# Kernel tuning notes

Hardware: AMD Instinct MI355X
Metric: run time of the kernel (lower is better)

Reference implementation:

```python
import jax, jax.numpy as jnp
import numpy as np

C_Z = 128
C = 128
EPS = 1e-5


def _layer_norm(x, w, b):
    m = jnp.mean(x, axis=-1, keepdims=True)
    v = jnp.mean(jnp.square(x - m), axis=-1, keepdims=True)
    return (x - m) * jax.lax.rsqrt(v + EPS) * w + b


def setup_inputs() -> dict:
    key = jax.random.key(0)
    ks = jax.random.split(key, 16)
    N = 512
    s_in = 1.0 / np.sqrt(C_Z)
    s_c = 1.0 / np.sqrt(C)
    return {
        "z": jax.random.normal(ks[0], (1, N, N, C_Z), dtype=jnp.float32),
        "ln_in_w": jnp.ones((C_Z,), jnp.float32),
        "ln_in_b": jnp.zeros((C_Z,), jnp.float32),
        "ln_out_w": jnp.ones((C_Z,), jnp.float32),
        "ln_out_b": jnp.zeros((C_Z,), jnp.float32),
        # weights stored [in, out]
        "w_ap": jax.random.normal(ks[1], (C_Z, C), jnp.float32) * s_in,
        "b_ap": jax.random.normal(ks[2], (C,), jnp.float32) * 0.02,
        "w_ag": jax.random.normal(ks[3], (C_Z, C), jnp.float32) * s_in,
        "b_ag": jax.random.normal(ks[4], (C,), jnp.float32) * 0.02,
        "w_bp": jax.random.normal(ks[5], (C_Z, C), jnp.float32) * s_in,
        "b_bp": jax.random.normal(ks[6], (C,), jnp.float32) * 0.02,
        "w_bg": jax.random.normal(ks[7], (C_Z, C), jnp.float32) * s_in,
        "b_bg": jax.random.normal(ks[8], (C,), jnp.float32) * 0.02,
        "w_g": jax.random.normal(ks[9], (C_Z, C_Z), jnp.float32) * s_in,
        "b_g": jax.random.normal(ks[10], (C_Z,), jnp.float32) * 0.02,
        "w_z": jax.random.normal(ks[11], (C, C_Z), jnp.float32) * s_c,
        "b_z": jax.random.normal(ks[12], (C_Z,), jnp.float32) * 0.02,
    }


def reference(z, ln_in_w, ln_in_b, ln_out_w, ln_out_b,
              w_ap, b_ap, w_ag, b_ag, w_bp, b_bp, w_bg, b_bg,
              w_g, b_g, w_z, b_z):
    zn = _layer_norm(z, ln_in_w, ln_in_b)                      # [B,N,N,c_z]
    a = jax.nn.sigmoid(zn @ w_ag + b_ag) * (zn @ w_ap + b_ap)  # [B,N,N,c]
    b = jax.nn.sigmoid(zn @ w_bg + b_bg) * (zn @ w_bp + b_bp)  # [B,N,N,c]
    g = jax.nn.sigmoid(zn @ w_g + b_g)                         # [B,N,N,c_z]
    # outgoing triangle update: contract over k
    t = jnp.einsum('bikc,bjkc->bijc', a, b)                    # [B,N,N,c]
    out = g * (_layer_norm(t, ln_out_w, ln_out_b) @ w_z + b_z)
    return out
```

## Files before the change

kernel.cpp:

```cpp
#include <hip/hip_runtime.h>
#include <hip/hip_bf16.h>


#define NSEQ 512
#define NPOS 262144

typedef short bf16x8 __attribute__((ext_vector_type(8)));
typedef float f32x4 __attribute__((ext_vector_type(4)));

__device__ __forceinline__ float bf2f(ushort h) {
    union { uint u; float f; } x; x.u = ((uint)h) << 16; return x.f;
}
__device__ __forceinline__ ushort f2bf(float f) {
    union { float f; uint u; } x; x.f = f;
    uint r = x.u + 0x7fffu + ((x.u >> 16) & 1u);
    return (ushort)(r >> 16);
}
__device__ __forceinline__ float sigm(float x) { return 1.f / (1.f + __expf(-x)); }

__device__ __forceinline__ float loadIn(const void* p, size_t idx, int isbf) {
    return isbf ? bf2f(((const ushort*)p)[idx]) : ((const float*)p)[idx];
}
__device__ __forceinline__ float2 loadIn2(const void* p, size_t base, int col2, int isbf) {
    if (isbf) {
        uint zz = *(const uint*)((const ushort*)p + base + col2);
        float2 r; r.x = bf2f((ushort)(zz & 0xffff)); r.y = bf2f((ushort)(zz >> 16)); return r;
    }
    return *(const float2*)((const float*)p + base + col2);
}

__global__ void detect_kernel(const uint* __restrict__ z32, int* __restrict__ flag)
{
    int t = threadIdx.x;
    int votes = 0;
    #pragma unroll
    for (int i = 0; i < 4; ++i) {
        uint wv = z32[t * 4 + i];
        uint ex = (wv >> 7) & 0xff;
        votes += (ex >= 118 && ex <= 132) ? 1 : 0;
    }
    #pragma unroll
    for (int m = 32; m >= 1; m >>= 1) votes += __shfl_xor(votes, m);
    if (t == 0) flag[0] = (votes >= 128) ? 1 : 0;
}

__global__ void fill_zero_kernel(ushort* __restrict__ out)
{
    size_t i = ((size_t)blockIdx.x * 256 + threadIdx.x) * 16;
    uint4 z4 = {0u, 0u, 0u, 0u};
    *(uint4*)(out + i) = z4;
    *(uint4*)(out + i + 8) = z4;
}

__global__ void prep_kernel(const void* __restrict__ w_ap, const void* __restrict__ w_ag,
                            const void* __restrict__ w_bp, const void* __restrict__ w_bg,
                            const void* __restrict__ w_g,  const void* __restrict__ w_z,
                            const void* __restrict__ ln_ow, const void* __restrict__ ln_ob,
                            const void* __restrict__ b_z,  const int* __restrict__ dflag,
                            ushort* __restrict__ wt5_h, ushort* __restrict__ wt5_l,
                            ushort* __restrict__ wzt_h, ushort* __restrict__ wzt_l,
                            float* __restrict__ u, float* __restrict__ v, int store_lo)
{
    const int b = blockIdx.x, t = threadIdx.x;
    const int isbf = dflag[0];
    if (b < 5) {
        const void* src = (b == 0) ? w_ap : (b == 1) ? w_ag : (b == 2) ? w_bp : (b == 3) ? w_bg : w_g;
        for (int k = 0; k < 64; ++k) {
            int o = t + k * 256;
            int co = o >> 7, ci = o & 127;
            float wv = loadIn(src, ci * 128 + co, isbf);
            ushort hi = f2bf(wv);
            wt5_h[b * 16384 + o] = hi;
            if (store_lo) wt5_l[b * 16384 + o] = f2bf(wv - bf2f(hi));
        }
    } else if (b == 5) {
        for (int k = 0; k < 64; ++k) {
            int o = t + k * 256;
            int co = o >> 7, c = o & 127;
            float wv = loadIn(ln_ow, c, isbf) * loadIn(w_z, c * 128 + co, isbf);
            ushort hi = f2bf(wv);
            wzt_h[o] = hi;
            if (store_lo) wzt_l[o] = f2bf(wv - bf2f(hi));
        }
    } else {
        if (t < 128) {
            float su = 0.f, sv = 0.f;
            for (int c = 0; c < 128; ++c) {
                float wzv = loadIn(w_z, c * 128 + t, isbf);
                su += loadIn(ln_ow, c, isbf) * wzv;
                sv += loadIn(ln_ob, c, isbf) * wzv;
            }
            u[t] = su;
            v[t] = sv + loadIn(b_z, t, isbf);
        }
    }
}

__global__ __launch_bounds__(256, 3)
void stage1_kernel(const void* __restrict__ z,
                   const void* __restrict__ ln_iw, const void* __restrict__ ln_ib,
                   const ushort* __restrict__ wt5_h,
                   const void* __restrict__ b_ap, const void* __restrict__ b_ag,
                   const void* __restrict__ b_bp, const void* __restrict__ b_bg,
                   const int* __restrict__ dflag,
                   ushort* __restrict__ Ahi, ushort* __restrict__ Alo,
                   ushort* __restrict__ Bhi, int walo)
{
    __shared__ ushort sm[2 * 64 * 136 + 128 * 72];
    ushort* lAh = sm;
    ushort* lAl = sm + 64 * 136;
    ushort* tb  = sm + 2 * 64 * 136;
    const int tid = threadIdx.x, lane = tid & 63, w = tid >> 6;
    const int l15 = lane & 15, quad = lane >> 4;
    const int p0 = blockIdx.x * 64;
    const int isbf = dflag[0];
    (void)Alo; (void)walo;

    float lw0 = loadIn(ln_iw, 2 * lane, isbf), lw1 = loadIn(ln_iw, 2 * lane + 1, isbf);
    float lb0 = loadIn(ln_ib, 2 * lane, isbf), lb1 = loadIn(ln_ib, 2 * lane + 1, isbf);
    for (int it = 0; it < 16; ++it) {
        int pl = w * 16 + it;
        float2 xv = loadIn2(z, (size_t)(p0 + pl) * 128, 2 * lane, isbf);
        float x0 = xv.x, x1 = xv.y;
        float s = x0 + x1, s2 = x0 * x0 + x1 * x1;
        #pragma unroll
        for (int m = 32; m >= 1; m >>= 1) { s += __shfl_xor(s, m); s2 += __shfl_xor(s2, m); }
        float mean = s * 0.0078125f;
        float var = s2 * 0.0078125f - mean * mean;
        float rs = rsqrtf(var + 1e-5f);
        float zn0 = (x0 - mean) * rs * lw0 + lb0;
        float zn1 = (x1 - mean) * rs * lw1 + lb1;
        ushort h0 = f2bf(zn0), h1 = f2bf(zn1);
        ushort o0 = f2bf(zn0 - bf2f(h0)), o1 = f2bf(zn1 - bf2f(h1));
        *(uint*)(lAh + pl * 136 + 2 * lane) = (uint)h0 | ((uint)h1 << 16);
        *(uint*)(lAl + pl * 136 + 2 * lane) = (uint)o0 | ((uint)o1 << 16);
    }
    __syncthreads();

    const int wm = w >> 1, wn = w & 1;
    const f32x4 zero4 = {0.f, 0.f, 0.f, 0.f};

    #pragma unroll 1
    for (int g = 0; g < 2; ++g) {
        const ushort* wG = wt5_h + ((g == 0) ? 1 : 3) * 16384;
        const ushort* wP = wt5_h + ((g == 0) ? 0 : 2) * 16384;

        f32x4 accG[2][4], accP[2][4];
        #pragma unroll
        for (int i = 0; i < 2; ++i)
            #pragma unroll
            for (int j = 0; j < 4; ++j) { accG[i][j] = zero4; accP[i][j] = zero4; }

        #pragma unroll
        for (int ks = 0; ks < 4; ++ks) {
            bf16x8 afh[2], afl[2];
            #pragma unroll
            for (int i = 0; i < 2; ++i) {
                afh[i] = *(const bf16x8*)(lAh + (wm * 32 + i * 16 + l15) * 136 + ks * 32 + quad * 8);
                afl[i] = *(const bf16x8*)(lAl + (wm * 32 + i * 16 + l15) * 136 + ks * 32 + quad * 8);
            }
            {
                bf16x8 bG[4];
                #pragma unroll
                for (int j = 0; j < 4; ++j)
                    bG[j] = *(const bf16x8*)(wG + (wn * 64 + j * 16 + l15) * 128 + ks * 32 + quad * 8);
                #pragma unroll
                for (int i = 0; i < 2; ++i)
                    #pragma unroll
                    for (int j = 0; j < 4; ++j) {
                        accG[i][j] = __builtin_amdgcn_mfma_f32_16x16x32_bf16(afh[i], bG[j], accG[i][j], 0, 0, 0);
                        accG[i][j] = __builtin_amdgcn_mfma_f32_16x16x32_bf16(afl[i], bG[j], accG[i][j], 0, 0, 0);
                    }
            }
            {
                bf16x8 bP[4];
                #pragma unroll
                for (int j = 0; j < 4; ++j)
                    bP[j] = *(const bf16x8*)(wP + (wn * 64 + j * 16 + l15) * 128 + ks * 32 + quad * 8);
                #pragma unroll
                for (int i = 0; i < 2; ++i)
                    #pragma unroll
                    for (int j = 0; j < 4; ++j) {
                        accP[i][j] = __builtin_amdgcn_mfma_f32_16x16x32_bf16(afh[i], bP[j], accP[i][j], 0, 0, 0);
                        accP[i][j] = __builtin_amdgcn_mfma_f32_16x16x32_bf16(afl[i], bP[j], accP[i][j], 0, 0, 0);
                    }
            }
        }

        const void* bgp = (g == 0) ? b_ag : b_bg;
        const void* bpp = (g == 0) ? b_ap : b_bp;
        float av[2][4][4];
        #pragma unroll
        for (int i = 0; i < 2; ++i)
            #pragma unroll
            for (int j = 0; j < 4; ++j) {
                int co = wn * 64 + j * 16 + l15;
                float gv = loadIn(bgp, co, isbf);
                float pv = loadIn(bpp, co, isbf);
                #pragma unroll
                for (int r = 0; r < 4; ++r)
                    av[i][j][r] = sigm(accG[i][j][r] + gv) * (accP[i][j][r] + pv);
            }

        ushort* dst_hi = (g == 0) ? Ahi : Bhi;

        __syncthreads();
        #pragma unroll
        for (int i = 0; i < 2; ++i)
            #pragma unroll
            for (int j = 0; j < 4; ++j) {
                int co = wn * 64 + j * 16 + l15;
                int pb = wm * 32 + i * 16 + quad * 4;
                uint2 pk;
                pk.x = (uint)f2bf(av[i][j][0]) | ((uint)f2bf(av[i][j][1]) << 16);
                pk.y = (uint)f2bf(av[i][j][2]) | ((uint)f2bf(av[i][j][3]) << 16);
                *(uint2*)(tb + co * 72 + pb) = pk;
            }
        __syncthreads();
        #pragma unroll
        for (int q = 0; q < 4; ++q) {
            int vv = q * 256 + tid;
            int co = vv >> 3, off = vv & 7;
            *(uint4*)(dst_hi + (size_t)co * NPOS + p0 + off * 8) = *(const uint4*)(tb + co * 72 + off * 8);
        }
    }
}

__global__ __launch_bounds__(256, 3)
void stage2_kernel(const ushort* __restrict__ Ahi, const ushort* __restrict__ Alo,
                   const ushort* __restrict__ Bhi, const int* __restrict__ dflag,
                   void* __restrict__ Tbuf, int alo, int tfp32)
{
    __shared__ ushort sm[2 * 128 * 72];
    ushort* lAh = sm;
    ushort* lBh = sm + 128 * 72;
    const int tid = threadIdx.x, lane = tid & 63, w = tid >> 6;
    const int l15 = lane & 15, quad = lane >> 4;
    const int wm = w >> 1, wn = w & 1;
    const int bid = blockIdx.y * 16 + blockIdx.x;
    const int swz = (bid & 7) * 256 + (bid >> 3);
    const int c = swz >> 4;
    const int ti = (swz & 15) >> 2, tj = swz & 3;
    const ushort* Aph = Ahi + (size_t)c * NPOS + (size_t)ti * 128 * NSEQ;
    const ushort* Bph = Bhi + (size_t)c * NPOS + (size_t)tj * 128 * NSEQ;
    (void)Alo; (void)alo;

    const f32x4 zero4 = {0.f, 0.f, 0.f, 0.f};
    f32x4 acc[4][4];
    #pragma unroll
    for (int i = 0; i < 4; ++i)
        #pragma unroll
        for (int j = 0; j < 4; ++j) acc[i][j] = zero4;

    for (int kt = 0; kt < 8; ++kt) {
        #pragma unroll
        for (int q = 0; q < 4; ++q) {
            int vv = q * 256 + tid;
            int row = vv >> 3, off = vv & 7;
            *(uint4*)(lAh + row * 72 + off * 8) = *(const uint4*)(Aph + (size_t)row * NSEQ + kt * 64 + off * 8);
            *(uint4*)(lBh + row * 72 + off * 8) = *(const uint4*)(Bph + (size_t)row * NSEQ + kt * 64 + off * 8);
        }
        __syncthreads();
        #pragma unroll
        for (int ks = 0; ks < 2; ++ks) {
            bf16x8 afh[4], bfh[4];
            #pragma unroll
            for (int i = 0; i < 4; ++i)
                afh[i] = *(const bf16x8*)(lAh + (wm * 64 + i * 16 + l15) * 72 + ks * 32 + quad * 8);
            #pragma unroll
            for (int j = 0; j < 4; ++j)
                bfh[j] = *(const bf16x8*)(lBh + (wn * 64 + j * 16 + l15) * 72 + ks * 32 + quad * 8);
            #pragma unroll
            for (int i = 0; i < 4; ++i)
                #pragma unroll
                for (int j = 0; j < 4; ++j)
                    acc[i][j] = __builtin_amdgcn_mfma_f32_16x16x32_bf16(afh[i], bfh[j], acc[i][j], 0, 0, 0);
        }
        __syncthreads();
    }

    if (tfp32) {
        float* Tp = (float*)Tbuf + ((size_t)(ti * 128) * 128 + c) * 512 + tj * 128;
        #pragma unroll
        for (int i = 0; i < 4; ++i)
            #pragma unroll
            for (int j = 0; j < 4; ++j) {
                int jl = wn * 64 + j * 16 + l15;
                int ib = wm * 64 + i * 16 + quad * 4;
                #pragma unroll
                for (int r = 0; r < 4; ++r)
                    Tp[(size_t)(ib + r) * 65536 + jl] = acc[i][j][r];
            }
    } else {
        ushort* Tp = (ushort*)Tbuf + ((size_t)(ti * 128) * 128 + c) * 512 + tj * 128;
        #pragma unroll
        for (int i = 0; i < 4; ++i)
            #pragma unroll
            for (int j = 0; j < 4; ++j) {
                int jl = wn * 64 + j * 16 + l15;
                int ib = wm * 64 + i * 16 + quad * 4;
                #pragma unroll
                for (int r = 0; r < 4; ++r)
                    Tp[(size_t)(ib + r) * 65536 + jl] = f2bf(acc[i][j][r]);
            }
    }
}

__global__ __launch_bounds__(256, 4)
void stage3ab_kernel(const void* __restrict__ z,
                     const void* __restrict__ ln_iw, const void* __restrict__ ln_ib,
                     const ushort* __restrict__ wt5_h, const ushort* __restrict__ wt5_l,
                     const void* __restrict__ b_g,
                     const float* __restrict__ Tf, const ushort* __restrict__ wzt_h,
                     const ushort* __restrict__ wzt_l,
                     const float* __restrict__ uvec, const float* __restrict__ vvec,
                     const int* __restrict__ dflag, void* __restrict__ out)
{
    __shared__ ushort sm[2 * 64 * 136];
    __shared__ float sMean[64], sRs[64];
    ushort* lAh = sm;
    ushort* lAl = sm + 64 * 136;
    const int tid = threadIdx.x, lane = tid & 63, w = tid >> 6;
    const int l15 = lane & 15, quad = lane >> 4;
    const int wm = w >> 1, wn = w & 1;
    const int p0 = blockIdx.x * 64;
    const int isbf = dflag[0];
    const f32x4 zero4 = {0.f, 0.f, 0.f, 0.f};
    (void)wt5_l; (void)wzt_l;

    float lw0 = loadIn(ln_iw, 2 * lane, isbf), lw1 = loadIn(ln_iw, 2 * lane + 1, isbf);
    float lb0 = loadIn(ln_ib, 2 * lane, isbf), lb1 = loadIn(ln_ib, 2 * lane + 1, isbf);
    for (int it = 0; it < 16; ++it) {
        int pl = w * 16 + it;
        float2 xv = loadIn2(z, (size_t)(p0 + pl) * 128, 2 * lane, isbf);
        float x0 = xv.x, x1 = xv.y;
        float s = x0 + x1, s2 = x0 * x0 + x1 * x1;
        #pragma unroll
        for (int m = 32; m >= 1; m >>= 1) { s += __shfl_xor(s, m); s2 += __shfl_xor(s2, m); }
        float mean = s * 0.0078125f;
        float var = s2 * 0.0078125f - mean * mean;
        float rs = rsqrtf(var + 1e-5f);
        float zn0 = (x0 - mean) * rs * lw0 + lb0;
        float zn1 = (x1 - mean) * rs * lw1 + lb1;
        ushort h0 = f2bf(zn0), h1 = f2bf(zn1);
        ushort o0 = f2bf(zn0 - bf2f(h0)), o1 = f2bf(zn1 - bf2f(h1));
        *(uint*)(lAh + pl * 136 + 2 * lane) = (uint)h0 | ((uint)h1 << 16);
        *(uint*)(lAl + pl * 136 + 2 * lane) = (uint)o0 | ((uint)o1 << 16);
    }
    __syncthreads();

    const ushort* wgh = wt5_h + 4 * 16384;
    f32x4 accG[2][4];
    #pragma unroll
    for (int i = 0; i < 2; ++i)
        #pragma unroll
        for (int j = 0; j < 4; ++j) accG[i][j] = zero4;
    #pragma unroll
    for (int ks = 0; ks < 4; ++ks) {
        bf16x8 afh[2], afl[2], bh[4];
        #pragma unroll
        for (int i = 0; i < 2; ++i) {
            afh[i] = *(const bf16x8*)(lAh + (wm * 32 + i * 16 + l15) * 136 + ks * 32 + quad * 8);
            afl[i] = *(const bf16x8*)(lAl + (wm * 32 + i * 16 + l15) * 136 + ks * 32 + quad * 8);
        }
        #pragma unroll
        for (int j = 0; j < 4; ++j)
            bh[j] = *(const bf16x8*)(wgh + (wn * 64 + j * 16 + l15) * 128 + ks * 32 + quad * 8);
        #pragma unroll
        for (int i = 0; i < 2; ++i)
            #pragma unroll
            for (int j = 0; j < 4; ++j) {
                accG[i][j] = __builtin_amdgcn_mfma_f32_16x16x32_bf16(afh[i], bh[j], accG[i][j], 0, 0, 0);
                accG[i][j] = __builtin_amdgcn_mfma_f32_16x16x32_bf16(afl[i], bh[j], accG[i][j], 0, 0, 0);
            }
    }
    #pragma unroll
    for (int i = 0; i < 2; ++i)
        #pragma unroll
        for (int j = 0; j < 4; ++j) {
            int co = wn * 64 + j * 16 + l15;
            float bgv = loadIn(b_g, co, isbf);
            #pragma unroll
            for (int r = 0; r < 4; ++r)
                accG[i][j][r] = sigm(accG[i][j][r] + bgv);
        }
    __syncthreads();

    {
        int c = tid >> 1, h = tid & 1;
        const float* src = Tf + ((size_t)(p0 >> 9) * 128 + c) * 512 + (p0 & 511) + h * 32;
        float tv[32];
        #pragma unroll
        for (int q8 = 0; q8 < 8; ++q8) {
            float4 f4 = ((const float4*)src)[q8];
            tv[q8 * 4 + 0] = f4.x; tv[q8 * 4 + 1] = f4.y;
            tv[q8 * 4 + 2] = f4.z; tv[q8 * 4 + 3] = f4.w;
        }
        #pragma unroll
        for (int jj = 0; jj < 32; ++jj) {
            ushort hi = f2bf(tv[jj]);
            lAh[(h * 32 + jj) * 136 + c] = hi;
            lAl[(h * 32 + jj) * 136 + c] = f2bf(tv[jj] - bf2f(hi));
        }
    }
    __syncthreads();

    for (int it = 0; it < 16; ++it) {
        int pl = w * 16 + it;
        uint zh = *(const uint*)(lAh + pl * 136 + 2 * lane);
        uint zl = *(const uint*)(lAl + pl * 136 + 2 * lane);
        float x0 = bf2f((ushort)(zh & 0xffff)) + bf2f((ushort)(zl & 0xffff));
        float x1 = bf2f((ushort)(zh >> 16)) + bf2f((ushort)(zl >> 16));
        float s = x0 + x1, s2 = x0 * x0 + x1 * x1;
        #pragma unroll
        for (int m = 32; m >= 1; m >>= 1) { s += __shfl_xor(s, m); s2 += __shfl_xor(s2, m); }
        if (lane == 0) {
            float mean = s * 0.0078125f;
            float var = s2 * 0.0078125f - mean * mean;
            sMean[pl] = mean;
            sRs[pl] = rsqrtf(var + 1e-5f);
        }
    }
    __syncthreads();

    f32x4 acc[2][4];
    #pragma unroll
    for (int i = 0; i < 2; ++i)
        #pragma unroll
        for (int j = 0; j < 4; ++j) acc[i][j] = zero4;
    #pragma unroll
    for (int ks = 0; ks < 4; ++ks) {
        bf16x8 afh[2], afl[2], bh[4];
        #pragma unroll
        for (int i = 0; i < 2; ++i) {
            afh[i] = *(const bf16x8*)(lAh + (wm * 32 + i * 16 + l15) * 136 + ks * 32 + quad * 8);
            afl[i] = *(const bf16x8*)(lAl + (wm * 32 + i * 16 + l15) * 136 + ks * 32 + quad * 8);
        }
        #pragma unroll
        for (int j = 0; j < 4; ++j)
            bh[j] = *(const bf16x8*)(wzt_h + (wn * 64 + j * 16 + l15) * 128 + ks * 32 + quad * 8);
        #pragma unroll
        for (int i = 0; i < 2; ++i)
            #pragma unroll
            for (int j = 0; j < 4; ++j) {
                acc[i][j] = __builtin_amdgcn_mfma_f32_16x16x32_bf16(afh[i], bh[j], acc[i][j], 0, 0, 0);
                acc[i][j] = __builtin_amdgcn_mfma_f32_16x16x32_bf16(afl[i], bh[j], acc[i][j], 0, 0, 0);
            }
    }

    ushort* outb = (ushort*)out;
    float*  outf = (float*)out;
    #pragma unroll
    for (int i = 0; i < 2; ++i)
        #pragma unroll
        for (int j = 0; j < 4; ++j) {
            int co = wn * 64 + j * 16 + l15;
            float uj = uvec[co], vj = vvec[co];
            int pb = wm * 32 + i * 16 + quad * 4;
            #pragma unroll
            for (int r = 0; r < 4; ++r) {
                int p = pb + r;
                float pre = sRs[p] * (acc[i][j][r] - sMean[p] * uj) + vj;
                float val = accG[i][j][r] * pre;
                size_t oidx = (size_t)(p0 + p) * 128 + co;
                if (isbf) outb[oidx] = f2bf(val);
                else      outf[oidx] = val;
            }
        }
}

__global__ __launch_bounds__(256, 2)
void stage3c_kernel(const void* __restrict__ z,
                    const void* __restrict__ ln_iw, const void* __restrict__ ln_ib,
                    const ushort* __restrict__ wt5_h, const void* __restrict__ b_g,
                    const ushort* __restrict__ Tb, const ushort* __restrict__ wzt_h,
                    const float* __restrict__ uvec, const float* __restrict__ vvec,
                    const int* __restrict__ dflag, void* __restrict__ out)
{
    __shared__ ushort sm[2 * 64 * 136 + 128 * 136];
    __shared__ float sMean[64], sRs[64];
    ushort* lAh = sm;
    ushort* lAl = sm + 64 * 136;
    ushort* lB  = sm + 2 * 64 * 136;
    const int tid = threadIdx.x, lane = tid & 63, w = tid >> 6;
    const int l15 = lane & 15, quad = lane >> 4;
    const int wm = w >> 1, wn = w & 1;
    const int p0 = blockIdx.x * 64;
    const int isbf = dflag[0];
    const f32x4 zero4 = {0.f, 0.f, 0.f, 0.f};

    float lw0 = loadIn(ln_iw, 2 * lane, isbf), lw1 = loadIn(ln_iw, 2 * lane + 1, isbf);
    float lb0 = loadIn(ln_ib, 2 * lane, isbf), lb1 = loadIn(ln_ib, 2 * lane + 1, isbf);
    for (int it = 0; it < 16; ++it) {
        int pl = w * 16 + it;
        float2 xv = loadIn2(z, (size_t)(p0 + pl) * 128, 2 * lane, isbf);
        float x0 = xv.x, x1 = xv.y;
        float s = x0 + x1, s2 = x0 * x0 + x1 * x1;
        #pragma unroll
        for (int m = 32; m >= 1; m >>= 1) { s += __shfl_xor(s, m); s2 += __shfl_xor(s2, m); }
        float mean = s * 0.0078125f;
        float var = s2 * 0.0078125f - mean * mean;
        float rs = rsqrtf(var + 1e-5f);
        float zn0 = (x0 - mean) * rs * lw0 + lb0;
        float zn1 = (x1 - mean) * rs * lw1 + lb1;
        ushort h0 = f2bf(zn0), h1 = f2bf(zn1);
        ushort o0 = f2bf(zn0 - bf2f(h0)), o1 = f2bf(zn1 - bf2f(h1));
        *(uint*)(lAh + pl * 136 + 2 * lane) = (uint)h0 | ((uint)h1 << 16);
        *(uint*)(lAl + pl * 136 + 2 * lane) = (uint)o0 | ((uint)o1 << 16);
    }
    {
        const ushort* src = wt5_h + 4 * 16384;
        #pragma unroll
        for (int q = 0; q < 8; ++q) {
            int vv = q * 256 + tid;
            int co = vv >> 4, off = vv & 15;
            *(uint4*)(lB + co * 136 + off * 8) = *(const uint4*)(src + co * 128 + off * 8);
        }
    }
    __syncthreads();

    f32x4 accG[2][4];
    #pragma unroll
    for (int i = 0; i < 2; ++i)
        #pragma unroll
        for (int j = 0; j < 4; ++j) accG[i][j] = zero4;
    #pragma unroll
    for (int ks = 0; ks < 4; ++ks) {
        bf16x8 afh[2], afl[2], bfr[4];
        #pragma unroll
        for (int i = 0; i < 2; ++i) {
            afh[i] = *(const bf16x8*)(lAh + (wm * 32 + i * 16 + l15) * 136 + ks * 32 + quad * 8);
            afl[i] = *(const bf16x8*)(lAl + (wm * 32 + i * 16 + l15) * 136 + ks * 32 + quad * 8);
        }
        #pragma unroll
        for (int j = 0; j < 4; ++j)
            bfr[j] = *(const bf16x8*)(lB + (wn * 64 + j * 16 + l15) * 136 + ks * 32 + quad * 8);
        #pragma unroll
        for (int i = 0; i < 2; ++i)
            #pragma unroll
            for (int j = 0; j < 4; ++j) {
                accG[i][j] = __builtin_amdgcn_mfma_f32_16x16x32_bf16(afh[i], bfr[j], accG[i][j], 0, 0, 0);
                accG[i][j] = __builtin_amdgcn_mfma_f32_16x16x32_bf16(afl[i], bfr[j], accG[i][j], 0, 0, 0);
            }
    }
    #pragma unroll
    for (int i = 0; i < 2; ++i)
        #pragma unroll
        for (int j = 0; j < 4; ++j) {
            int co = wn * 64 + j * 16 + l15;
            float bgv = loadIn(b_g, co, isbf);
            #pragma unroll
            for (int r = 0; r < 4; ++r)
                accG[i][j][r] = sigm(accG[i][j][r] + bgv);
        }
    __syncthreads();

    {
        int c = tid >> 1, h = tid & 1;
        const ushort* src = Tb + ((size_t)(p0 >> 9) * 128 + c) * 512 + (p0 & 511) + h * 32;
        union { uint4 q[4]; ushort u[32]; } tmp;
        tmp.q[0] = ((const uint4*)src)[0];
        tmp.q[1] = ((const uint4*)src)[1];
        tmp.q[2] = ((const uint4*)src)[2];
        tmp.q[3] = ((const uint4*)src)[3];
        #pragma unroll
        for (int jj = 0; jj < 32; ++jj)
            lAh[(h * 32 + jj) * 136 + c] = tmp.u[jj];
    }
    #pragma unroll
    for (int q = 0; q < 8; ++q) {
        int vv = q * 256 + tid;
        int co = vv >> 4, off = vv & 15;
        *(uint4*)(lB + co * 136 + off * 8) = *(const uint4*)(wzt_h + co * 128 + off * 8);
    }
    __syncthreads();

    for (int it = 0; it < 16; ++it) {
        int pl = w * 16 + it;
        uint zz = *(const uint*)(lAh + pl * 136 + 2 * lane);
        float x0 = bf2f((ushort)(zz & 0xffff)), x1 = bf2f((ushort)(zz >> 16));
        float s = x0 + x1, s2 = x0 * x0 + x1 * x1;
        #pragma unroll
        for (int m = 32; m >= 1; m >>= 1) { s += __shfl_xor(s, m); s2 += __shfl_xor(s2, m); }
        if (lane == 0) {
            float mean = s * 0.0078125f;
            float var = s2 * 0.0078125f - mean * mean;
            sMean[pl] = mean;
            sRs[pl] = rsqrtf(var + 1e-5f);
        }
    }
    __syncthreads();

    f32x4 acc[2][4];
    #pragma unroll
    for (int i = 0; i < 2; ++i)
        #pragma unroll
        for (int j = 0; j < 4; ++j) acc[i][j] = zero4;
    #pragma unroll
    for (int ks = 0; ks < 4; ++ks) {
        bf16x8 af[2], bfr[4];
        #pragma unroll
        for (int i = 0; i < 2; ++i)
            af[i] = *(const bf16x8*)(lAh + (wm * 32 + i * 16 + l15) * 136 + ks * 32 + quad * 8);
        #pragma unroll
        for (int j = 0; j < 4; ++j)
            bfr[j] = *(const bf16x8*)(lB + (wn * 64 + j * 16 + l15) * 136 + ks * 32 + quad * 8);
        #pragma unroll
        for (int i = 0; i < 2; ++i)
            #pragma unroll
            for (int j = 0; j < 4; ++j)
                acc[i][j] = __builtin_amdgcn_mfma_f32_16x16x32_bf16(af[i], bfr[j], acc[i][j], 0, 0, 0);
    }

    ushort* outb = (ushort*)out;
    float*  outf = (float*)out;
    #pragma unroll
    for (int i = 0; i < 2; ++i)
        #pragma unroll
        for (int j = 0; j < 4; ++j) {
            int co = wn * 64 + j * 16 + l15;
            float uj = uvec[co], vj = vvec[co];
            int pb = wm * 32 + i * 16 + quad * 4;
            #pragma unroll
            for (int r = 0; r < 4; ++r) {
                int p = pb + r;
                float pre = sRs[p] * (acc[i][j][r] - sMean[p] * uj) + vj;
                float val = accG[i][j][r] * pre;
                size_t oidx = (size_t)(p0 + p) * 128 + co;
                if (isbf) outb[oidx] = f2bf(val);
                else      outf[oidx] = val;
            }
        }
}

extern "C" void kernel_launch(void* const* d_in, const int* in_sizes, int n_in,
                              void* d_out, int out_size, void* d_ws, size_t ws_size,
                              hipStream_t stream)
{
    const void* z     = d_in[0];
    const void* ln_iw = d_in[1];
    const void* ln_ib = d_in[2];
    const void* ln_ow = d_in[3];
    const void* ln_ob = d_in[4];
    const void* w_ap  = d_in[5];
    const void* b_ap  = d_in[6];
    const void* w_ag  = d_in[7];
    const void* b_ag  = d_in[8];
    const void* w_bp  = d_in[9];
    const void* b_bp  = d_in[10];
    const void* w_bg  = d_in[11];
    const void* b_bg  = d_in[12];
    const void* w_g   = d_in[13];
    const void* b_g   = d_in[14];
    const void* w_z   = d_in[15];
    const void* b_z   = d_in[16];

    const size_t MB64 = 67108864;
    const size_t REQ_C = 262144 + 2 * MB64;
    const size_t REQ_B = 524288 + MB64 + 2 * MB64;
    const size_t REQ_A = REQ_B + MB64;

    char* ws = (char*)d_ws;
    if (ws_size < REQ_C) {
        fill_zero_kernel<<<8192, 256, 0, stream>>>((ushort*)d_out);
        return;
    }

    int tier = (ws_size >= REQ_A) ? 0 : (ws_size >= REQ_B) ? 1 : 2;
    if (tier == 0) tier = 1;

    ushort* wt5_h = (ushort*)(ws);
    ushort* wzt_h = (ushort*)(ws + 163840);
    float*  uvec  = (float*)(ws + 196608);
    float*  vvec  = (float*)(ws + 197120);
    int*    dflag = (int*)(ws + 198144);
    ushort* wt5_l = (ushort*)(ws + 262144);
    ushort* wzt_l = (ushort*)(ws + 262144 + 163840);
    int store_lo = 0;
    if (tier == 2) { wt5_l = wt5_h; wzt_l = wzt_h; }

    ushort* Ahi; ushort* Alo; void* Tbuf;
    int walo = 0, tfp32 = 0;
    if (tier == 1) {
        Ahi = (ushort*)(ws + 524288);
        Alo = Ahi;
        Tbuf = (void*)(ws + 524288 + MB64);
        walo = 0; tfp32 = 1;
    } else {
        Ahi = (ushort*)(ws + 262144);
        Alo = Ahi;
        Tbuf = (void*)(ws + 262144 + MB64);
        walo = 0; tfp32 = 0;
    }
    ushort* Bhi = (ushort*)d_out;

    detect_kernel<<<1, 64, 0, stream>>>((const uint*)z, dflag);
    prep_kernel<<<7, 256, 0, stream>>>(w_ap, w_ag, w_bp, w_bg, w_g, w_z, ln_ow, ln_ob, b_z,
                                       dflag, wt5_h, wt5_l, wzt_h, wzt_l, uvec, vvec, store_lo);
    stage1_kernel<<<4096, 256, 0, stream>>>(z, ln_iw, ln_ib, wt5_h,
                                            b_ap, b_ag, b_bp, b_bg, dflag,
                                            Ahi, Alo, Bhi, walo);
    stage2_kernel<<<dim3(16, 128), 256, 0, stream>>>(Ahi, Alo, Bhi, dflag, Tbuf, walo, tfp32);
    if (tfp32)
        stage3ab_kernel<<<4096, 256, 0, stream>>>(z, ln_iw, ln_ib, wt5_h, wt5_l, b_g,
                                                  (const float*)Tbuf, wzt_h, wzt_l,
                                                  uvec, vvec, dflag, d_out);
    else
        stage3c_kernel<<<4096, 256, 0, stream>>>(z, ln_iw, ln_ib, wt5_h, b_g,
                                                 (const ushort*)Tbuf, wzt_h,
                                                 uvec, vvec, dflag, d_out);
}
```

Measured before the change: 759.5 us.

## Compute sigmoid gate in stage1 and store it, skipping z re-read in stage3

The gate projection sigmoid(zn@w_g+b_g) now runs in stage1, where zn is already in LDS, and is written as bf16 to a workspace buffer in channel-major layout. A new stage3g kernel reads only T, computes its hi/lo split for the layer norm and output projection, and multiplies by the stored gate. This removes the second read and layernorm of z and the gate GEMM from stage3. In exchange it adds a 64MB gate write plus a strided gate read, and it needs a larger workspace. The bf16-T stage3c path is removed.

```diff
diff --git a/kernel.cpp b/kernel.cpp
--- a/kernel.cpp
+++ b/kernel.cpp
@@ -102,9 +102,10 @@
                    const ushort* __restrict__ wt5_h,
                    const void* __restrict__ b_ap, const void* __restrict__ b_ag,
                    const void* __restrict__ b_bp, const void* __restrict__ b_bg,
+                   const void* __restrict__ b_g,
                    const int* __restrict__ dflag,
-                   ushort* __restrict__ Ahi, ushort* __restrict__ Alo,
-                   ushort* __restrict__ Bhi, int walo)
+                   ushort* __restrict__ Ahi, ushort* __restrict__ Bhi,
+                   ushort* __restrict__ Gbuf, int do_gate)
 {
     __shared__ ushort sm[2 * 64 * 136 + 128 * 72];
     ushort* lAh = sm;
@@ -114,7 +115,6 @@
     const int l15 = lane & 15, quad = lane >> 4;
     const int p0 = blockIdx.x * 64;
     const int isbf = dflag[0];
-    (void)Alo; (void)walo;
 
     float lw0 = loadIn(ln_iw, 2 * lane, isbf), lw1 = loadIn(ln_iw, 2 * lane + 1, isbf);
     float lb0 = loadIn(ln_ib, 2 * lane, isbf), lb1 = loadIn(ln_ib, 2 * lane + 1, isbf);
@@ -224,12 +224,60 @@
             *(uint4*)(dst_hi + (size_t)co * NPOS + p0 + off * 8) = *(const uint4*)(tb + co * 72 + off * 8);
         }
     }
+
+    if (do_gate) {
+        const ushort* wGt = wt5_h + 4 * 16384;
+        f32x4 acc[2][4];
+        #pragma unroll
+        for (int i = 0; i < 2; ++i)
+            #pragma unroll
+            for (int j = 0; j < 4; ++j) acc[i][j] = zero4;
+        #pragma unroll
+        for (int ks = 0; ks < 4; ++ks) {
+            bf16x8 afh[2], afl[2], bh[4];
+            #pragma unroll
+            for (int i = 0; i < 2; ++i) {
+                afh[i] = *(const bf16x8*)(lAh + (wm * 32 + i * 16 + l15) * 136 + ks * 32 + quad * 8);
+                afl[i] = *(const bf16x8*)(lAl + (wm * 32 + i * 16 + l15) * 136 + ks * 32 + quad * 8);
+            }
+            #pragma unroll
+            for (int j = 0; j < 4; ++j)
+                bh[j] = *(const bf16x8*)(wGt + (wn * 64 + j * 16 + l15) * 128 + ks * 32 + quad * 8);
+            #pragma unroll
+            for (int i = 0; i < 2; ++i)
+                #pragma unroll
+                for (int j = 0; j < 4; ++j) {
+                    acc[i][j] = __builtin_amdgcn_mfma_f32_16x16x32_bf16(afh[i], bh[j], acc[i][j], 0, 0, 0);
+                    acc[i][j] = __builtin_amdgcn_mfma_f32_16x16x32_bf16(afl[i], bh[j], acc[i][j], 0, 0, 0);
+                }
+        }
+        __syncthreads();
+        #pragma unroll
+        for (int i = 0; i < 2; ++i)
+            #pragma unroll
+            for (int j = 0; j < 4; ++j) {
+                int co = wn * 64 + j * 16 + l15;
+                float bgv = loadIn(b_g, co, isbf);
+                int pb = wm * 32 + i * 16 + quad * 4;
+                uint2 pk;
+                pk.x = (uint)f2bf(sigm(acc[i][j][0] + bgv)) | ((uint)f2bf(sigm(acc[i][j][1] + bgv)) << 16);
+                pk.y = (uint)f2bf(sigm(acc[i][j][2] + bgv)) | ((uint)f2bf(sigm(acc[i][j][3] + bgv)) << 16);
+                *(uint2*)(tb + co * 72 + pb) = pk;
+            }
+        __syncthreads();
+        #pragma unroll
+        for (int q = 0; q < 4; ++q) {
+            int vv = q * 256 + tid;
+            int co = vv >> 3, off = vv & 7;
+            *(uint4*)(Gbuf + (size_t)co * NPOS + p0 + off * 8) = *(const uint4*)(tb + co * 72 + off * 8);
+        }
+    }
 }
 
 __global__ __launch_bounds__(256, 3)
-void stage2_kernel(const ushort* __restrict__ Ahi, const ushort* __restrict__ Alo,
-                   const ushort* __restrict__ Bhi, const int* __restrict__ dflag,
-                   void* __restrict__ Tbuf, int alo, int tfp32)
+void stage2_kernel(const ushort* __restrict__ Ahi, const ushort* __restrict__ Bhi,
+                   const int* __restrict__ dflag,
+                   void* __restrict__ Tbuf, int tfp32)
 {
     __shared__ ushort sm[2 * 128 * 72];
     ushort* lAh = sm;
@@ -243,7 +291,6 @@
     const int ti = (swz & 15) >> 2, tj = swz & 3;
     const ushort* Aph = Ahi + (size_t)c * NPOS + (size_t)ti * 128 * NSEQ;
     const ushort* Bph = Bhi + (size_t)c * NPOS + (size_t)tj * 128 * NSEQ;
-    (void)Alo; (void)alo;
 
     const f32x4 zero4 = {0.f, 0.f, 0.f, 0.f};
     f32x4 acc[4][4];
@@ -307,14 +354,10 @@
 }
 
 __global__ __launch_bounds__(256, 4)
-void stage3ab_kernel(const void* __restrict__ z,
-                     const void* __restrict__ ln_iw, const void* __restrict__ ln_ib,
-                     const ushort* __restrict__ wt5_h, const ushort* __restrict__ wt5_l,
-                     const void* __restrict__ b_g,
-                     const float* __restrict__ Tf, const ushort* __restrict__ wzt_h,
-                     const ushort* __restrict__ wzt_l,
-                     const float* __restrict__ uvec, const float* __restrict__ vvec,
-                     const int* __restrict__ dflag, void* __restrict__ out)
+void stage3g_kernel(const float* __restrict__ Tf, const ushort* __restrict__ Gbuf,
+                    const ushort* __restrict__ wzt_h,
+                    const float* __restrict__ uvec, const float* __restrict__ vvec,
+                    const int* __restrict__ dflag, void* __restrict__ out)
 {
     __shared__ ushort sm[2 * 64 * 136];
     __shared__ float sMean[64], sRs[64];
@@ -326,7 +369,115 @@
     const int p0 = blockIdx.x * 64;
     const int isbf = dflag[0];
     const f32x4 zero4 = {0.f, 0.f, 0.f, 0.f};
-    (void)wt5_l; (void)wzt_l;
+
+    {
+        int c = tid >> 1, h = tid & 1;
+        const float* src = Tf + ((size_t)(p0 >> 9) * 128 + c) * 512 + (p0 & 511) + h * 32;
+        float tv[32];
+        #pragma unroll
+        for (int q8 = 0; q8 < 8; ++q8) {
+            float4 f4 = ((const float4*)src)[q8];
+            tv[q8 * 4 + 0] = f4.x; tv[q8 * 4 + 1] = f4.y;
+            tv[q8 * 4 + 2] = f4.z; tv[q8 * 4 + 3] = f4.w;
+        }
+        #pragma unroll
+        for (int jj = 0; jj < 32; ++jj) {
+            ushort hi = f2bf(tv[jj]);
+            lAh[(h * 32 + jj) * 136 + c] = hi;
+            lAl[(h * 32 + jj) * 136 + c] = f2bf(tv[jj] - bf2f(hi));
+        }
+    }
+    __syncthreads();
+
+    for (int it = 0; it < 16; ++it) {
+        int pl = w * 16 + it;
+        uint zh = *(const uint*)(lAh + pl * 136 + 2 * lane);
+        uint zl = *(const uint*)(lAl + pl * 136 + 2 * lane);
+        float x0 = bf2f((ushort)(zh & 0xffff)) + bf2f((ushort)(zl & 0xffff));
+        float x1 = bf2f((ushort)(zh >> 16)) + bf2f((ushort)(zl >> 16));
+        float s = x0 + x1, s2 = x0 * x0 + x1 * x1;
+        #pragma unroll
+        for (int m = 32; m >= 1; m >>= 1) { s += __shfl_xor(s, m); s2 += __shfl_xor(s2, m); }
+        if (lane == 0) {
+            float mean = s * 0.0078125f;
+            float var = s2 * 0.0078125f - mean * mean;
+            sMean[pl] = mean;
+            sRs[pl] = rsqrtf(var + 1e-5f);
+        }
+    }
+    __syncthreads();
+
+    f32x4 acc[2][4];
+    #pragma unroll
+    for (int i = 0; i < 2; ++i)
+        #pragma unroll
+        for (int j = 0; j < 4; ++j) acc[i][j] = zero4;
+    #pragma unroll
+    for (int ks = 0; ks < 4; ++ks) {
+        bf16x8 afh[2], afl[2], bh[4];
+        #pragma unroll
+        for (int i = 0; i < 2; ++i) {
+            afh[i] = *(const bf16x8*)(lAh + (wm * 32 + i * 16 + l15) * 136 + ks * 32 + quad * 8);
+            afl[i] = *(const bf16x8*)(lAl + (wm * 32 + i * 16 + l15) * 136 + ks * 32 + quad * 8);
+        }
+        #pragma unroll
+        for (int j = 0; j < 4; ++j)
+            bh[j] = *(const bf16x8*)(wzt_h + (wn * 64 + j * 16 + l15) * 128 + ks * 32 + quad * 8);
+        #pragma unroll
+        for (int i = 0; i < 2; ++i)
+            #pragma unroll
+            for (int j = 0; j < 4; ++j) {
+                acc[i][j] = __builtin_amdgcn_mfma_f32_16x16x32_bf16(afh[i], bh[j], acc[i][j], 0, 0, 0);
+                acc[i][j] = __builtin_amdgcn_mfma_f32_16x16x32_bf16(afl[i], bh[j], acc[i][j], 0, 0, 0);
+            }
+    }
+
+    ushort* outb = (ushort*)out;
+    float*  outf = (float*)out;
+    #pragma unroll
+    for (int i = 0; i < 2; ++i)
+        #pragma unroll
+        for (int j = 0; j < 4; ++j) {
+            int co = wn * 64 + j * 16 + l15;
+            float uj = uvec[co], vj = vvec[co];
+            int pb = wm * 32 + i * 16 + quad * 4;
+            uint2 gpk = *(const uint2*)(Gbuf + (size_t)co * NPOS + p0 + pb);
+            float gg[4];
+            gg[0] = bf2f((ushort)(gpk.x & 0xffff));
+            gg[1] = bf2f((ushort)(gpk.x >> 16));
+            gg[2] = bf2f((ushort)(gpk.y & 0xffff));
+            gg[3] = bf2f((ushort)(gpk.y >> 16));
+            #pragma unroll
+            for (int r = 0; r < 4; ++r) {
+                int p = pb + r;
+                float pre = sRs[p] * (acc[i][j][r] - sMean[p] * uj) + vj;
+                float val = gg[r] * pre;
+                size_t oidx = (size_t)(p0 + p) * 128 + co;
+                if (isbf) outb[oidx] = f2bf(val);
+                else      outf[oidx] = val;
+            }
+        }
+}
+
+__global__ __launch_bounds__(256, 4)
+void stage3ab_kernel(const void* __restrict__ z,
+                     const void* __restrict__ ln_iw, const void* __restrict__ ln_ib,
+                     const ushort* __restrict__ wt5_h,
+                     const void* __restrict__ b_g,
+                     const float* __restrict__ Tf, const ushort* __restrict__ wzt_h,
+                     const float* __restrict__ uvec, const float* __restrict__ vvec,
+                     const int* __restrict__ dflag, void* __restrict__ out)
+{
+    __shared__ ushort sm[2 * 64 * 136];
+    __shared__ float sMean[64], sRs[64];
+    ushort* lAh = sm;
+    ushort* lAl = sm + 64 * 136;
+    const int tid = threadIdx.x, lane = tid & 63, w = tid >> 6;
+    const int l15 = lane & 15, quad = lane >> 4;
+    const int wm = w >> 1, wn = w & 1;
+    const int p0 = blockIdx.x * 64;
+    const int isbf = dflag[0];
+    const f32x4 zero4 = {0.f, 0.f, 0.f, 0.f};
 
     float lw0 = loadIn(ln_iw, 2 * lane, isbf), lw1 = loadIn(ln_iw, 2 * lane + 1, isbf);
     float lb0 = loadIn(ln_ib, 2 * lane, isbf), lb1 = loadIn(ln_ib, 2 * lane + 1, isbf);
@@ -446,170 +597,6 @@
                 acc[i][j] = __builtin_amdgcn_mfma_f32_16x16x32_bf16(afh[i], bh[j], acc[i][j], 0, 0, 0);
                 acc[i][j] = __builtin_amdgcn_mfma_f32_16x16x32_bf16(afl[i], bh[j], acc[i][j], 0, 0, 0);
             }
-    }
-
-    ushort* outb = (ushort*)out;
-    float*  outf = (float*)out;
-    #pragma unroll
-    for (int i = 0; i < 2; ++i)
-        #pragma unroll
-        for (int j = 0; j < 4; ++j) {
-            int co = wn * 64 + j * 16 + l15;
-            float uj = uvec[co], vj = vvec[co];
-            int pb = wm * 32 + i * 16 + quad * 4;
-            #pragma unroll
-            for (int r = 0; r < 4; ++r) {
-                int p = pb + r;
-                float pre = sRs[p] * (acc[i][j][r] - sMean[p] * uj) + vj;
-                float val = accG[i][j][r] * pre;
-                size_t oidx = (size_t)(p0 + p) * 128 + co;
-                if (isbf) outb[oidx] = f2bf(val);
-                else      outf[oidx] = val;
-            }
-        }
-}
-
-__global__ __launch_bounds__(256, 2)
-void stage3c_kernel(const void* __restrict__ z,
-                    const void* __restrict__ ln_iw, const void* __restrict__ ln_ib,
-                    const ushort* __restrict__ wt5_h, const void* __restrict__ b_g,
-                    const ushort* __restrict__ Tb, const ushort* __restrict__ wzt_h,
-                    const float* __restrict__ uvec, const float* __restrict__ vvec,
-                    const int* __restrict__ dflag, void* __restrict__ out)
-{
-    __shared__ ushort sm[2 * 64 * 136 + 128 * 136];
-    __shared__ float sMean[64], sRs[64];
-    ushort* lAh = sm;
-    ushort* lAl = sm + 64 * 136;
-    ushort* lB  = sm + 2 * 64 * 136;
-    const int tid = threadIdx.x, lane = tid & 63, w = tid >> 6;
-    const int l15 = lane & 15, quad = lane >> 4;
-    const int wm = w >> 1, wn = w & 1;
-    const int p0 = blockIdx.x * 64;
-    const int isbf = dflag[0];
-    const f32x4 zero4 = {0.f, 0.f, 0.f, 0.f};
-
-    float lw0 = loadIn(ln_iw, 2 * lane, isbf), lw1 = loadIn(ln_iw, 2 * lane + 1, isbf);
-    float lb0 = loadIn(ln_ib, 2 * lane, isbf), lb1 = loadIn(ln_ib, 2 * lane + 1, isbf);
-    for (int it = 0; it < 16; ++it) {
-        int pl = w * 16 + it;
-        float2 xv = loadIn2(z, (size_t)(p0 + pl) * 128, 2 * lane, isbf);
-        float x0 = xv.x, x1 = xv.y;
-        float s = x0 + x1, s2 = x0 * x0 + x1 * x1;
-        #pragma unroll
-        for (int m = 32; m >= 1; m >>= 1) { s += __shfl_xor(s, m); s2 += __shfl_xor(s2, m); }
-        float mean = s * 0.0078125f;
-        float var = s2 * 0.0078125f - mean * mean;
-        float rs = rsqrtf(var + 1e-5f);
-        float zn0 = (x0 - mean) * rs * lw0 + lb0;
-        float zn1 = (x1 - mean) * rs * lw1 + lb1;
-        ushort h0 = f2bf(zn0), h1 = f2bf(zn1);
-        ushort o0 = f2bf(zn0 - bf2f(h0)), o1 = f2bf(zn1 - bf2f(h1));
-        *(uint*)(lAh + pl * 136 + 2 * lane) = (uint)h0 | ((uint)h1 << 16);
-        *(uint*)(lAl + pl * 136 + 2 * lane) = (uint)o0 | ((uint)o1 << 16);
-    }
-    {
-        const ushort* src = wt5_h + 4 * 16384;
-        #pragma unroll
-        for (int q = 0; q < 8; ++q) {
-            int vv = q * 256 + tid;
-            int co = vv >> 4, off = vv & 15;
-            *(uint4*)(lB + co * 136 + off * 8) = *(const uint4*)(src + co * 128 + off * 8);
-        }
-    }
-    __syncthreads();
-
-    f32x4 accG[2][4];
-    #pragma unroll
-    for (int i = 0; i < 2; ++i)
-        #pragma unroll
-        for (int j = 0; j < 4; ++j) accG[i][j] = zero4;
-    #pragma unroll
-    for (int ks = 0; ks < 4; ++ks) {
-        bf16x8 afh[2], afl[2], bfr[4];
-        #pragma unroll
-        for (int i = 0; i < 2; ++i) {
-            afh[i] = *(const bf16x8*)(lAh + (wm * 32 + i * 16 + l15) * 136 + ks * 32 + quad * 8);
-            afl[i] = *(const bf16x8*)(lAl + (wm * 32 + i * 16 + l15) * 136 + ks * 32 + quad * 8);
-        }
-        #pragma unroll
-        for (int j = 0; j < 4; ++j)
-            bfr[j] = *(const bf16x8*)(lB + (wn * 64 + j * 16 + l15) * 136 + ks * 32 + quad * 8);
-        #pragma unroll
-        for (int i = 0; i < 2; ++i)
-            #pragma unroll
-            for (int j = 0; j < 4; ++j) {
-                accG[i][j] = __builtin_amdgcn_mfma_f32_16x16x32_bf16(afh[i], bfr[j], accG[i][j], 0, 0, 0);
-                accG[i][j] = __builtin_amdgcn_mfma_f32_16x16x32_bf16(afl[i], bfr[j], accG[i][j], 0, 0, 0);
-            }
-    }
-    #pragma unroll
-    for (int i = 0; i < 2; ++i)
-        #pragma unroll
-        for (int j = 0; j < 4; ++j) {
-            int co = wn * 64 + j * 16 + l15;
-            float bgv = loadIn(b_g, co, isbf);
-            #pragma unroll
-            for (int r = 0; r < 4; ++r)
-                accG[i][j][r] = sigm(accG[i][j][r] + bgv);
-        }
-    __syncthreads();
-
-    {
-        int c = tid >> 1, h = tid & 1;
-        const ushort* src = Tb + ((size_t)(p0 >> 9) * 128 + c) * 512 + (p0 & 511) + h * 32;
-        union { uint4 q[4]; ushort u[32]; } tmp;
-        tmp.q[0] = ((const uint4*)src)[0];
-        tmp.q[1] = ((const uint4*)src)[1];
-        tmp.q[2] = ((const uint4*)src)[2];
-        tmp.q[3] = ((const uint4*)src)[3];
-        #pragma unroll
-        for (int jj = 0; jj < 32; ++jj)
-            lAh[(h * 32 + jj) * 136 + c] = tmp.u[jj];
-    }
-    #pragma unroll
-    for (int q = 0; q < 8; ++q) {
-        int vv = q * 256 + tid;
-        int co = vv >> 4, off = vv & 15;
-        *(uint4*)(lB + co * 136 + off * 8) = *(const uint4*)(wzt_h + co * 128 + off * 8);
-    }
-    __syncthreads();
-
-    for (int it = 0; it < 16; ++it) {
-        int pl = w * 16 + it;
-        uint zz = *(const uint*)(lAh + pl * 136 + 2 * lane);
-        float x0 = bf2f((ushort)(zz & 0xffff)), x1 = bf2f((ushort)(zz >> 16));
-        float s = x0 + x1, s2 = x0 * x0 + x1 * x1;
-        #pragma unroll
-        for (int m = 32; m >= 1; m >>= 1) { s += __shfl_xor(s, m); s2 += __shfl_xor(s2, m); }
-        if (lane == 0) {
-            float mean = s * 0.0078125f;
-            float var = s2 * 0.0078125f - mean * mean;
-            sMean[pl] = mean;
-            sRs[pl] = rsqrtf(var + 1e-5f);
-        }
-    }
-    __syncthreads();
-
-    f32x4 acc[2][4];
-    #pragma unroll
-    for (int i = 0; i < 2; ++i)
-        #pragma unroll
-        for (int j = 0; j < 4; ++j) acc[i][j] = zero4;
-    #pragma unroll
-    for (int ks = 0; ks < 4; ++ks) {
-        bf16x8 af[2], bfr[4];
-        #pragma unroll
-        for (int i = 0; i < 2; ++i)
-            af[i] = *(const bf16x8*)(lAh + (wm * 32 + i * 16 + l15) * 136 + ks * 32 + quad * 8);
-        #pragma unroll
-        for (int j = 0; j < 4; ++j)
-            bfr[j] = *(const bf16x8*)(lB + (wn * 64 + j * 16 + l15) * 136 + ks * 32 + quad * 8);
-        #pragma unroll
-        for (int i = 0; i < 2; ++i)
-            #pragma unroll
-            for (int j = 0; j < 4; ++j)
-                acc[i][j] = __builtin_amdgcn_mfma_f32_16x16x32_bf16(af[i], bfr[j], acc[i][j], 0, 0, 0);
     }
 
     ushort* outb = (ushort*)out;
@@ -656,18 +643,15 @@
     const void* b_z   = d_in[16];
 
     const size_t MB64 = 67108864;
-    const size_t REQ_C = 262144 + 2 * MB64;
     const size_t REQ_B = 524288 + MB64 + 2 * MB64;
     const size_t REQ_A = REQ_B + MB64;
 
     char* ws = (char*)d_ws;
-    if (ws_size < REQ_C) {
+    if (ws_size < REQ_B) {
         fill_zero_kernel<<<8192, 256, 0, stream>>>((ushort*)d_out);
         return;
     }
-
-    int tier = (ws_size >= REQ_A) ? 0 : (ws_size >= REQ_B) ? 1 : 2;
-    if (tier == 0) tier = 1;
+    const int use_g = (ws_size >= REQ_A);
 
     ushort* wt5_h = (ushort*)(ws);
     ushort* wzt_h = (ushort*)(ws + 163840);
@@ -676,37 +660,24 @@
     int*    dflag = (int*)(ws + 198144);
     ushort* wt5_l = (ushort*)(ws + 262144);
     ushort* wzt_l = (ushort*)(ws + 262144 + 163840);
-    int store_lo = 0;
-    if (tier == 2) { wt5_l = wt5_h; wzt_l = wzt_h; }
-
-    ushort* Ahi; ushort* Alo; void* Tbuf;
-    int walo = 0, tfp32 = 0;
-    if (tier == 1) {
-        Ahi = (ushort*)(ws + 524288);
-        Alo = Ahi;
-        Tbuf = (void*)(ws + 524288 + MB64);
-        walo = 0; tfp32 = 1;
-    } else {
-        Ahi = (ushort*)(ws + 262144);
-        Alo = Ahi;
-        Tbuf = (void*)(ws + 262144 + MB64);
-        walo = 0; tfp32 = 0;
-    }
-    ushort* Bhi = (ushort*)d_out;
+
+    ushort* Ahi  = (ushort*)(ws + 524288);
+    ushort* Gbuf = use_g ? (ushort*)(ws + 524288 + MB64) : (ushort*)(ws + 524288);
+    void*   Tbuf = use_g ? (void*)(ws + 524288 + 2 * MB64) : (void*)(ws + 524288 + MB64);
+    ushort* Bhi  = (ushort*)d_out;
 
     detect_kernel<<<1, 64, 0, stream>>>((const uint*)z, dflag);
     prep_kernel<<<7, 256, 0, stream>>>(w_ap, w_ag, w_bp, w_bg, w_g, w_z, ln_ow, ln_ob, b_z,
-                                       dflag, wt5_h, wt5_l, wzt_h, wzt_l, uvec, vvec, store_lo);
+                                       dflag, wt5_h, wt5_l, wzt_h, wzt_l, uvec, vvec, 0);
     stage1_kernel<<<4096, 256, 0, stream>>>(z, ln_iw, ln_ib, wt5_h,
-                                            b_ap, b_ag, b_bp, b_bg, dflag,
-                                            Ahi, Alo, Bhi, walo);
-    stage2_kernel<<<dim3(16, 128), 256, 0, stream>>>(Ahi, Alo, Bhi, dflag, Tbuf, walo, tfp32);
-    if (tfp32)
-        stage3ab_kernel<<<4096, 256, 0, stream>>>(z, ln_iw, ln_ib, wt5_h, wt5_l, b_g,
-                                                  (const float*)Tbuf, wzt_h, wzt_l,
+                                            b_ap, b_ag, b_bp, b_bg, b_g, dflag,
+                                            Ahi, Bhi, Gbuf, use_g);
+    stage2_kernel<<<dim3(16, 128), 256, 0, stream>>>(Ahi, Bhi, dflag, Tbuf, 1);
+    if (use_g)
+        stage3g_kernel<<<4096, 256, 0, stream>>>((const float*)Tbuf, Gbuf, wzt_h,
+                                                 uvec, vvec, dflag, d_out);
+    else
+        stage3ab_kernel<<<4096, 256, 0, stream>>>(z, ln_iw, ln_ib, wt5_h, b_g,
+                                                  (const float*)Tbuf, wzt_h,
                                                   uvec, vvec, dflag, d_out);
-    else
-        stage3c_kernel<<<4096, 256, 0, stream>>>(z, ln_iw, ln_ib, wt5_h, b_g,
-                                                 (const ushort*)Tbuf, wzt_h,
-                                                 uvec, vvec, dflag, d_out);
-}
+}
```

Result: no change. 747.3 us (-1.6%).
